# Performance work log

Hardware: AMD Instinct MI355X
Metric: run time of the kernel (lower is better)

## Reference

```python
import jax, jax.numpy as jnp
import numpy as np

N, F, K, D = 4096, 512, 8, 64
NEG_MIN = jnp.finfo(jnp.float32).min  # tf.float32.min used as additive mask


def setup_inputs() -> dict:
    key = jax.random.key(0)
    k1, k2, k3, k4, k5, k6 = jax.random.split(key, 6)
    H = jax.random.normal(k1, (N, F), dtype=jnp.float32)
    # binary adjacency as float (original multiplies (1 - A) by float32.min)
    A = jax.random.randint(k2, (N, N), 0, 2).astype(jnp.float32)
    idx = jnp.arange(N, dtype=jnp.int32)
    W = jax.random.normal(k3, (K, F, D), dtype=jnp.float32) * 0.05
    b = jax.random.normal(k4, (K, D), dtype=jnp.float32) * 0.05
    attn_k1 = jax.random.normal(k5, (K, D), dtype=jnp.float32) * 0.05
    attn_k2 = jax.random.normal(k6, (K, D), dtype=jnp.float32) * 0.05
    return {"H": H, "A": A, "idx": idx, "W": W, "b": b,
            "attn_k1": attn_k1, "attn_k2": attn_k2}


def reference(H, A, idx, W, b, attn_k1, attn_k2):
    # batch_A = gather(A, idx, axis=1); idx = arange(N) -> full adjacency
    batch_A = A[:, idx]                                   # [N, N]
    # all K heads at once (heads are independent, identical math)
    HW = jnp.einsum('nf,kfd->knd', H, W)                  # [K, N, D]
    s1 = jnp.einsum('knd,kd->kn', HW, attn_k1)            # [K, N]
    s2 = jnp.einsum('knd,kd->kn', HW, attn_k2)            # [K, N]
    # tf.meshgrid + transpose => attn[i, j] = s1[i] + s2[j]
    attn = s1[:, :, None] + s2[:, None, :]                # [K, N, N]
    attn = attn + NEG_MIN * (1.0 - batch_A)               # additive adjacency mask
    attn = jnp.where(attn > 0, attn, 0.2 * attn)          # LeakyReLU(0.2) AFTER mask
    attn = jax.nn.softmax(attn, axis=-1)                  # rows sum to 1
    # dropout layers are identity at inference (training=False)
    res = jnp.einsum('knm,kmd->knd', attn, HW) + b[:, None, :]
    res = jax.nn.relu(res)                                # activation per head (is_last=False)
    # concat heads along feature axis -> [N, K*D]
    return jnp.transpose(res, (1, 0, 2)).reshape(N, K * D)
```

## Files before the change

kernel.cpp:

```cpp
#include <hip/hip_runtime.h>
#include <hip/hip_bf16.h>

#define NN 4096
#define FF 512
#define KK 8
#define DD 64

typedef __attribute__((ext_vector_type(8))) short bf16x8;
typedef __attribute__((ext_vector_type(4))) float f32x4;

static __device__ __forceinline__ unsigned int cvt_pk_bf16(float lo, float hi) {
    unsigned int r;
    asm("v_cvt_pk_bf16_f32 %0, %1, %2" : "=v"(r) : "v"(lo), "v"(hi));
    return r;
}

__global__ __launch_bounds__(256) void pack_mask_k(const float* __restrict__ A,
                                                   unsigned int* __restrict__ Abits) {
    int w = blockIdx.x * 256 + threadIdx.x;
    const float4* src = (const float4*)(A + (size_t)w * 32);
    unsigned int bits = 0u;
#pragma unroll
    for (int i = 0; i < 8; ++i) {
        float4 v = src[i];
        bits |= (v.x != 0.f ? 1u : 0u) << (i * 4 + 0);
        bits |= (v.y != 0.f ? 1u : 0u) << (i * 4 + 1);
        bits |= (v.z != 0.f ? 1u : 0u) << (i * 4 + 2);
        bits |= (v.w != 0.f ? 1u : 0u) << (i * 4 + 3);
    }
    Abits[w] = bits;
}

__global__ __launch_bounds__(256) void cvt_h_k(const float* __restrict__ H,
                                               uint4* __restrict__ Hb4) {
    int i = blockIdx.x * 256 + threadIdx.x;
    float4 a = ((const float4*)H)[i * 2];
    float4 b = ((const float4*)H)[i * 2 + 1];
    uint4 v;
    v.x = cvt_pk_bf16(a.x, a.y);
    v.y = cvt_pk_bf16(a.z, a.w);
    v.z = cvt_pk_bf16(b.x, b.y);
    v.w = cvt_pk_bf16(b.z, b.w);
    Hb4[i] = v;
}

__global__ __launch_bounds__(256) void cvt_wt_k(const float* __restrict__ W,
                                                ushort* __restrict__ WT) {
    int k = blockIdx.x, f0 = blockIdx.y * 64;
    __shared__ float lds[64][65];
    const float* src = W + ((size_t)k * FF + f0) * DD;
    int t = threadIdx.x;
#pragma unroll
    for (int i = 0; i < 4; ++i) {
        int idx4 = t + i * 256;
        int f = idx4 >> 4, d4 = (idx4 & 15) * 4;
        float4 v = *(const float4*)(src + (size_t)f * DD + d4);
        lds[f][d4 + 0] = v.x; lds[f][d4 + 1] = v.y;
        lds[f][d4 + 2] = v.z; lds[f][d4 + 3] = v.w;
    }
    __syncthreads();
    int d = t >> 2, fs = (t & 3) * 16;
    ushort* dst = WT + ((size_t)k * DD + d) * FF + f0 + fs;
    uint4 v0, v1;
    v0.x = cvt_pk_bf16(lds[fs + 0][d], lds[fs + 1][d]);
    v0.y = cvt_pk_bf16(lds[fs + 2][d], lds[fs + 3][d]);
    v0.z = cvt_pk_bf16(lds[fs + 4][d], lds[fs + 5][d]);
    v0.w = cvt_pk_bf16(lds[fs + 6][d], lds[fs + 7][d]);
    v1.x = cvt_pk_bf16(lds[fs + 8][d], lds[fs + 9][d]);
    v1.y = cvt_pk_bf16(lds[fs + 10][d], lds[fs + 11][d]);
    v1.z = cvt_pk_bf16(lds[fs + 12][d], lds[fs + 13][d]);
    v1.w = cvt_pk_bf16(lds[fs + 14][d], lds[fs + 15][d]);
    *(uint4*)dst = v0;
    *(uint4*)(dst + 8) = v1;
}

__global__ __launch_bounds__(256) void hw_mfma_k(const ushort* __restrict__ Hb,
                                                 const ushort* __restrict__ WT,
                                                 const float* __restrict__ ak1,
                                                 const float* __restrict__ ak2,
                                                 float* __restrict__ r1,
                                                 float* __restrict__ E2,
                                                 float* __restrict__ e2p,
                                                 ushort* __restrict__ HWT2) {
    int k = blockIdx.x;
    int wrow = blockIdx.y * 64 + (threadIdx.x >> 6) * 16;
    int l = threadIdx.x & 63;
    int lr = l & 15, lg = l >> 4;

    f32x4 acc[4];
#pragma unroll
    for (int f = 0; f < 4; ++f) acc[f] = (f32x4){0.f, 0.f, 0.f, 0.f};

    const ushort* ha = Hb + (size_t)(wrow + lr) * FF + lg * 8;
    const ushort* wa = WT + (size_t)(k * DD + lr) * FF + lg * 8;
#pragma unroll 4
    for (int f0 = 0; f0 < FF; f0 += 32) {
        bf16x8 a = *(const bf16x8*)(ha + f0);
#pragma unroll
        for (int f = 0; f < 4; ++f) {
            bf16x8 b = *(const bf16x8*)(wa + (size_t)f * 16 * FF + f0);
            acc[f] = __builtin_amdgcn_mfma_f32_16x16x32_bf16(a, b, acc[f], 0, 0, 0);
        }
    }

    float p1[4] = {0.f, 0.f, 0.f, 0.f}, p2[4] = {0.f, 0.f, 0.f, 0.f};
#pragma unroll
    for (int f = 0; f < 4; ++f) {
        float a1 = ak1[k * DD + f * 16 + lr];
        float a2 = ak2[k * DD + f * 16 + lr];
#pragma unroll
        for (int i = 0; i < 4; ++i) {
            p1[i] = fmaf(acc[f][i], a1, p1[i]);
            p2[i] = fmaf(acc[f][i], a2, p2[i]);
        }
    }
#pragma unroll
    for (int off = 1; off < 16; off <<= 1) {
#pragma unroll
        for (int i = 0; i < 4; ++i) {
            p1[i] += __shfl_xor(p1[i], off);
            p2[i] += __shfl_xor(p2[i], off);
        }
    }
    if (lr == 0) {
#pragma unroll
        for (int i = 0; i < 4; ++i) {
            int n = k * NN + wrow + lg * 4 + i;
            r1[n]  = __expf(-0.8f * p1[i]);
            E2[n]  = __expf(p2[i]);
            e2p[n] = __expf(0.2f * p2[i]);
        }
    }
    size_t basei = ((size_t)(k * 512 + (wrow >> 3) + (lg >> 1))) * 512
                 + (size_t)lr * 8 + (lg & 1) * 4;
#pragma unroll
    for (int f = 0; f < 4; ++f) {
        uint2 v;
        v.x = cvt_pk_bf16(acc[f][0], acc[f][1]);
        v.y = cvt_pk_bf16(acc[f][2], acc[f][3]);
        *(uint2*)&HWT2[basei + (size_t)f * 128] = v;
    }
}

__global__ __launch_bounds__(256) void attn_pv_f(const ushort* __restrict__ HWT2,
                                                 const float* __restrict__ r1v,
                                                 const float* __restrict__ E2v,
                                                 const float* __restrict__ e2pv,
                                                 const unsigned char* __restrict__ Ab8,
                                                 const float* __restrict__ bias,
                                                 float* __restrict__ out) {
    int b = blockIdx.x;
    int k = b & 7;
    int row0 = (b >> 3) * 32;

    int w = threadIdx.x >> 6;
    int l = threadIdx.x & 63;
    int lr = l & 15, lg = l >> 4;

    __shared__ float tb[8192];
    __shared__ float ps[4][32];

    {
        const float4* e2s = (const float4*)(E2v + (size_t)k * NN);
        const float4* qps = (const float4*)(e2pv + (size_t)k * NN);
        float4* t4p = (float4*)tb;
#pragma unroll
        for (int n = 0; n < 4; ++n) {
            t4p[threadIdx.x + n * 256]        = e2s[threadIdx.x + n * 256];
            t4p[1024 + threadIdx.x + n * 256] = qps[threadIdx.x + n * 256];
        }
    }
    __syncthreads();

    float r1r0 = r1v[k * NN + row0 + lr];
    float r1r1 = r1v[k * NN + row0 + 16 + lr];
    const uint4* mrow0 = (const uint4*)(Ab8 + (size_t)(row0 + lr) * (NN / 8) + w * 128);
    const uint4* mrow1 = (const uint4*)(Ab8 + (size_t)(row0 + 16 + lr) * (NN / 8) + w * 128);
    const ushort* hwg = HWT2 + ((size_t)(k * 512 + w * 128 + lg)) * 512 + (size_t)lr * 8;
    const float* tE = tb + w * 1024 + lg * 8;
    const float* tQ = tb + 4096 + w * 1024 + lg * 8;

    bf16x8 onesb;
#pragma unroll
    for (int j = 0; j < 8; ++j) onesb[j] = (lr == 0) ? (short)0x3F80 : (short)0;

    f32x4 acc0[4], acc1[4];
#pragma unroll
    for (int f = 0; f < 4; ++f) {
        acc0[f] = (f32x4){0.f, 0.f, 0.f, 0.f};
        acc1[f] = (f32x4){0.f, 0.f, 0.f, 0.f};
    }
    f32x4 accs0 = (f32x4){0.f, 0.f, 0.f, 0.f};
    f32x4 accs1 = (f32x4){0.f, 0.f, 0.f, 0.f};

    bf16x8 bb[2][4];
#pragma unroll
    for (int f = 0; f < 4; ++f) bb[0][f] = *(const bf16x8*)(hwg + f * 128);

    for (int t4 = 0; t4 < 8; ++t4) {
        uint4 mu0 = mrow0[t4], mu1 = mrow1[t4];
        unsigned int mw0[4] = {mu0.x, mu0.y, mu0.z, mu0.w};
        unsigned int mw1[4] = {mu1.x, mu1.y, mu1.z, mu1.w};
#pragma unroll
        for (int j = 0; j < 4; ++j) {
            int it = t4 * 4 + j;
            const int cur = j & 1, nxt = cur ^ 1;
            int itn = it + 1 - ((it + 1) >> 5);
#pragma unroll
            for (int f = 0; f < 4; ++f)
                bb[nxt][f] = *(const bf16x8*)(hwg + (size_t)itn * 2048 + f * 128);
            const float* ltE = tE + it * 32;
            const float* ltQ = tQ + it * 32;
            float4 ea = *(const float4*)(ltE), eb = *(const float4*)(ltE + 4);
            float4 qa = *(const float4*)(ltQ), qb = *(const float4*)(ltQ + 4);
            float ev[8] = {ea.x, ea.y, ea.z, ea.w, eb.x, eb.y, eb.z, eb.w};
            float qv[8] = {qa.x, qa.y, qa.z, qa.w, qb.x, qb.y, qb.z, qb.w};
            unsigned int mb0 = (mw0[j] >> (lg * 8)) & 0xffu;
            unsigned int mb1 = (mw1[j] >> (lg * 8)) & 0xffu;
            uint4 au0, au1;
            unsigned int* pu0 = &au0.x;
            unsigned int* pu1 = &au1.x;
#pragma unroll
            for (int p = 0; p < 4; ++p) {
                int ja = 2 * p, jb = 2 * p + 1;
                unsigned int m0a = (unsigned int)(((int)(mb0 << (31 - ja))) >> 31);
                unsigned int m0b = (unsigned int)(((int)(mb0 << (31 - jb))) >> 31);
                unsigned int m1a = (unsigned int)(((int)(mb1 << (31 - ja))) >> 31);
                unsigned int m1b = (unsigned int)(((int)(mb1 << (31 - jb))) >> 31);
                float y0a = fmaxf(ev[ja], r1r0 * qv[ja]);
                float y0b = fmaxf(ev[jb], r1r0 * qv[jb]);
                float y1a = fmaxf(ev[ja], r1r1 * qv[ja]);
                float y1b = fmaxf(ev[jb], r1r1 * qv[jb]);
                y0a = __uint_as_float(__float_as_uint(y0a) & m0a);
                y0b = __uint_as_float(__float_as_uint(y0b) & m0b);
                y1a = __uint_as_float(__float_as_uint(y1a) & m1a);
                y1b = __uint_as_float(__float_as_uint(y1b) & m1b);
                pu0[p] = cvt_pk_bf16(y0a, y0b);
                pu1[p] = cvt_pk_bf16(y1a, y1b);
            }
            bf16x8 af0 = __builtin_bit_cast(bf16x8, au0);
            bf16x8 af1 = __builtin_bit_cast(bf16x8, au1);
            accs0 = __builtin_amdgcn_mfma_f32_16x16x32_bf16(af0, onesb, accs0, 0, 0, 0);
            accs1 = __builtin_amdgcn_mfma_f32_16x16x32_bf16(af1, onesb, accs1, 0, 0, 0);
#pragma unroll
            for (int f = 0; f < 4; ++f) {
                acc0[f] = __builtin_amdgcn_mfma_f32_16x16x32_bf16(af0, bb[cur][f], acc0[f], 0, 0, 0);
                acc1[f] = __builtin_amdgcn_mfma_f32_16x16x32_bf16(af1, bb[cur][f], acc1[f], 0, 0, 0);
            }
        }
    }

    __syncthreads();
#pragma unroll
    for (int f = 0; f < 4; ++f)
#pragma unroll
        for (int i = 0; i < 4; ++i) {
            tb[w * 2048 + (lg * 4 + i) * 64 + f * 16 + lr]      = acc0[f][i];
            tb[w * 2048 + (16 + lg * 4 + i) * 64 + f * 16 + lr] = acc1[f][i];
        }
    if (lr == 0) {
#pragma unroll
        for (int i = 0; i < 4; ++i) {
            ps[w][lg * 4 + i]      = accs0[i];
            ps[w][16 + lg * 4 + i] = accs1[i];
        }
    }
    __syncthreads();

    const float4* red4 = (const float4*)tb;
#pragma unroll
    for (int j2 = 0; j2 < 2; ++j2) {
        int o4 = threadIdx.x + j2 * 256;
        int row = o4 >> 4, d4 = (o4 & 15) * 4;
        float4 s0 = red4[o4], s1_ = red4[512 + o4];
        float4 s2_ = red4[1024 + o4], s3 = red4[1536 + o4];
        float rs = ps[0][row] + ps[1][row] + ps[2][row] + ps[3][row];
        float inv = 1.f / rs;
        float4 bi = *(const float4*)(bias + k * DD + d4);
        float4 o;
        o.x = fmaxf(fmaf(s0.x + s1_.x + s2_.x + s3.x, inv, bi.x), 0.f);
        o.y = fmaxf(fmaf(s0.y + s1_.y + s2_.y + s3.y, inv, bi.y), 0.f);
        o.z = fmaxf(fmaf(s0.z + s1_.z + s2_.z + s3.z, inv, bi.z), 0.f);
        o.w = fmaxf(fmaf(s0.w + s1_.w + s2_.w + s3.w, inv, bi.w), 0.f);
        *(float4*)&out[(size_t)(row0 + row) * (KK * DD) + k * DD + d4] = o;
    }
}

extern "C" void kernel_launch(void* const* d_in, const int* in_sizes, int n_in,
                              void* d_out, int out_size, void* d_ws, size_t ws_size,
                              hipStream_t stream) {
    const float* H   = (const float*)d_in[0];
    const float* A   = (const float*)d_in[1];
    const float* W   = (const float*)d_in[3];
    const float* b   = (const float*)d_in[4];
    const float* ak1 = (const float*)d_in[5];
    const float* ak2 = (const float*)d_in[6];
    float* out = (float*)d_out;

    char* ws = (char*)d_ws;
    size_t off = 0;
    ushort* Hb   = (ushort*)(ws + off); off += (size_t)NN * FF * 2;
    ushort* HWT2 = (ushort*)(ws + off); off += (size_t)KK * DD * NN * 2;
    ushort* WT   = (ushort*)(ws + off); off += (size_t)KK * DD * FF * 2;
    unsigned int* Abits = (unsigned int*)(ws + off); off += (size_t)NN * NN / 8;
    float* r1  = (float*)(ws + off); off += (size_t)KK * NN * 4;
    float* E2  = (float*)(ws + off); off += (size_t)KK * NN * 4;
    float* e2p = (float*)(ws + off); off += (size_t)KK * NN * 4;

    pack_mask_k<<<dim3(NN * (NN / 32) / 256), 256, 0, stream>>>(A, Abits);
    cvt_h_k<<<dim3(NN * FF / 8 / 256), 256, 0, stream>>>(H, (uint4*)Hb);
    cvt_wt_k<<<dim3(KK, FF / 64), 256, 0, stream>>>(W, WT);
    hw_mfma_k<<<dim3(KK, NN / 64), 256, 0, stream>>>(Hb, WT, ak1, ak2,
                                                     r1, E2, e2p, HWT2);
    attn_pv_f<<<dim3(KK * (NN / 32)), 256, 0, stream>>>(
        HWT2, r1, E2, e2p, (const unsigned char*)Abits, b, out);
}
```

Before: 78.29 us.

## Merge prep kernels into two launches and raise MFMA wave priority

Combines the H and W bf16 conversion kernels into one launch, and folds the adjacency bit-packing into the HW GEMM launch as extra blocks so the mask packing runs concurrently with the projection GEMM. This cuts launch count from five to three and lets the memory-bound mask pass overlap with compute-bound MFMA work. It also wraps the attention kernel's MFMA block with s_setprio to favor issuing matrix ops. Risks include block-level divergence in the merged kernels and scheduling interactions from the priority change.

```diff
diff --git a/kernel.cpp b/kernel.cpp
--- a/kernel.cpp
+++ b/kernel.cpp
@@ -15,75 +15,79 @@
     return r;
 }
 
-__global__ __launch_bounds__(256) void pack_mask_k(const float* __restrict__ A,
+__global__ __launch_bounds__(256) void prep_cvt_k(const float* __restrict__ H,
+                                                  const float* __restrict__ W,
+                                                  uint4* __restrict__ Hb4,
+                                                  ushort* __restrict__ WT) {
+    __shared__ float lds[64][65];
+    int bid = blockIdx.x;
+    int t = threadIdx.x;
+    if (bid < 1024) {
+        int i = bid * 256 + t;
+        float4 a = ((const float4*)H)[i * 2];
+        float4 b = ((const float4*)H)[i * 2 + 1];
+        uint4 v;
+        v.x = cvt_pk_bf16(a.x, a.y);
+        v.y = cvt_pk_bf16(a.z, a.w);
+        v.z = cvt_pk_bf16(b.x, b.y);
+        v.w = cvt_pk_bf16(b.z, b.w);
+        Hb4[i] = v;
+    } else {
+        int k = (bid - 1024) >> 3, f0 = ((bid - 1024) & 7) * 64;
+        const float* src = W + ((size_t)k * FF + f0) * DD;
+#pragma unroll
+        for (int i = 0; i < 4; ++i) {
+            int idx4 = t + i * 256;
+            int f = idx4 >> 4, d4 = (idx4 & 15) * 4;
+            float4 v = *(const float4*)(src + (size_t)f * DD + d4);
+            lds[f][d4 + 0] = v.x; lds[f][d4 + 1] = v.y;
+            lds[f][d4 + 2] = v.z; lds[f][d4 + 3] = v.w;
+        }
+        __syncthreads();
+        int d = t >> 2, fs = (t & 3) * 16;
+        ushort* dst = WT + ((size_t)k * DD + d) * FF + f0 + fs;
+        uint4 v0, v1;
+        v0.x = cvt_pk_bf16(lds[fs + 0][d], lds[fs + 1][d]);
+        v0.y = cvt_pk_bf16(lds[fs + 2][d], lds[fs + 3][d]);
+        v0.z = cvt_pk_bf16(lds[fs + 4][d], lds[fs + 5][d]);
+        v0.w = cvt_pk_bf16(lds[fs + 6][d], lds[fs + 7][d]);
+        v1.x = cvt_pk_bf16(lds[fs + 8][d], lds[fs + 9][d]);
+        v1.y = cvt_pk_bf16(lds[fs + 10][d], lds[fs + 11][d]);
+        v1.z = cvt_pk_bf16(lds[fs + 12][d], lds[fs + 13][d]);
+        v1.w = cvt_pk_bf16(lds[fs + 14][d], lds[fs + 15][d]);
+        *(uint4*)dst = v0;
+        *(uint4*)(dst + 8) = v1;
+    }
+}
+
+__global__ __launch_bounds__(256) void gemm_pack_k(const ushort* __restrict__ Hb,
+                                                   const ushort* __restrict__ WT,
+                                                   const float* __restrict__ ak1,
+                                                   const float* __restrict__ ak2,
+                                                   const float* __restrict__ A,
+                                                   float* __restrict__ r1,
+                                                   float* __restrict__ E2,
+                                                   float* __restrict__ e2p,
+                                                   ushort* __restrict__ HWT2,
                                                    unsigned int* __restrict__ Abits) {
-    int w = blockIdx.x * 256 + threadIdx.x;
-    const float4* src = (const float4*)(A + (size_t)w * 32);
-    unsigned int bits = 0u;
-#pragma unroll
-    for (int i = 0; i < 8; ++i) {
-        float4 v = src[i];
-        bits |= (v.x != 0.f ? 1u : 0u) << (i * 4 + 0);
-        bits |= (v.y != 0.f ? 1u : 0u) << (i * 4 + 1);
-        bits |= (v.z != 0.f ? 1u : 0u) << (i * 4 + 2);
-        bits |= (v.w != 0.f ? 1u : 0u) << (i * 4 + 3);
-    }
-    Abits[w] = bits;
-}
-
-__global__ __launch_bounds__(256) void cvt_h_k(const float* __restrict__ H,
-                                               uint4* __restrict__ Hb4) {
-    int i = blockIdx.x * 256 + threadIdx.x;
-    float4 a = ((const float4*)H)[i * 2];
-    float4 b = ((const float4*)H)[i * 2 + 1];
-    uint4 v;
-    v.x = cvt_pk_bf16(a.x, a.y);
-    v.y = cvt_pk_bf16(a.z, a.w);
-    v.z = cvt_pk_bf16(b.x, b.y);
-    v.w = cvt_pk_bf16(b.z, b.w);
-    Hb4[i] = v;
-}
-
-__global__ __launch_bounds__(256) void cvt_wt_k(const float* __restrict__ W,
-                                                ushort* __restrict__ WT) {
-    int k = blockIdx.x, f0 = blockIdx.y * 64;
-    __shared__ float lds[64][65];
-    const float* src = W + ((size_t)k * FF + f0) * DD;
-    int t = threadIdx.x;
-#pragma unroll
-    for (int i = 0; i < 4; ++i) {
-        int idx4 = t + i * 256;
-        int f = idx4 >> 4, d4 = (idx4 & 15) * 4;
-        float4 v = *(const float4*)(src + (size_t)f * DD + d4);
-        lds[f][d4 + 0] = v.x; lds[f][d4 + 1] = v.y;
-        lds[f][d4 + 2] = v.z; lds[f][d4 + 3] = v.w;
-    }
-    __syncthreads();
-    int d = t >> 2, fs = (t & 3) * 16;
-    ushort* dst = WT + ((size_t)k * DD + d) * FF + f0 + fs;
-    uint4 v0, v1;
-    v0.x = cvt_pk_bf16(lds[fs + 0][d], lds[fs + 1][d]);
-    v0.y = cvt_pk_bf16(lds[fs + 2][d], lds[fs + 3][d]);
-    v0.z = cvt_pk_bf16(lds[fs + 4][d], lds[fs + 5][d]);
-    v0.w = cvt_pk_bf16(lds[fs + 6][d], lds[fs + 7][d]);
-    v1.x = cvt_pk_bf16(lds[fs + 8][d], lds[fs + 9][d]);
-    v1.y = cvt_pk_bf16(lds[fs + 10][d], lds[fs + 11][d]);
-    v1.z = cvt_pk_bf16(lds[fs + 12][d], lds[fs + 13][d]);
-    v1.w = cvt_pk_bf16(lds[fs + 14][d], lds[fs + 15][d]);
-    *(uint4*)dst = v0;
-    *(uint4*)(dst + 8) = v1;
-}
-
-__global__ __launch_bounds__(256) void hw_mfma_k(const ushort* __restrict__ Hb,
-                                                 const ushort* __restrict__ WT,
-                                                 const float* __restrict__ ak1,
-                                                 const float* __restrict__ ak2,
-                                                 float* __restrict__ r1,
-                                                 float* __restrict__ E2,
-                                                 float* __restrict__ e2p,
-                                                 ushort* __restrict__ HWT2) {
-    int k = blockIdx.x;
-    int wrow = blockIdx.y * 64 + (threadIdx.x >> 6) * 16;
+    int bid = blockIdx.x;
+    if (bid >= 512) {
+        int w = (bid - 512) * 256 + threadIdx.x;
+        const float4* src = (const float4*)(A + (size_t)w * 32);
+        unsigned int bits = 0u;
+#pragma unroll
+        for (int i = 0; i < 8; ++i) {
+            float4 v = src[i];
+            bits |= (v.x != 0.f ? 1u : 0u) << (i * 4 + 0);
+            bits |= (v.y != 0.f ? 1u : 0u) << (i * 4 + 1);
+            bits |= (v.z != 0.f ? 1u : 0u) << (i * 4 + 2);
+            bits |= (v.w != 0.f ? 1u : 0u) << (i * 4 + 3);
+        }
+        Abits[w] = bits;
+        return;
+    }
+    int k = bid & 7;
+    int wrow = (bid >> 3) * 64 + (threadIdx.x >> 6) * 16;
     int l = threadIdx.x & 63;
     int lr = l & 15, lg = l >> 4;
 
@@ -240,6 +244,7 @@
             }
             bf16x8 af0 = __builtin_bit_cast(bf16x8, au0);
             bf16x8 af1 = __builtin_bit_cast(bf16x8, au1);
+            __builtin_amdgcn_s_setprio(1);
             accs0 = __builtin_amdgcn_mfma_f32_16x16x32_bf16(af0, onesb, accs0, 0, 0, 0);
             accs1 = __builtin_amdgcn_mfma_f32_16x16x32_bf16(af1, onesb, accs1, 0, 0, 0);
 #pragma unroll
@@ -247,6 +252,7 @@
                 acc0[f] = __builtin_amdgcn_mfma_f32_16x16x32_bf16(af0, bb[cur][f], acc0[f], 0, 0, 0);
                 acc1[f] = __builtin_amdgcn_mfma_f32_16x16x32_bf16(af1, bb[cur][f], acc1[f], 0, 0, 0);
             }
+            __builtin_amdgcn_s_setprio(0);
         }
     }
 
@@ -307,11 +313,9 @@
     float* E2  = (float*)(ws + off); off += (size_t)KK * NN * 4;
     float* e2p = (float*)(ws + off); off += (size_t)KK * NN * 4;
 
-    pack_mask_k<<<dim3(NN * (NN / 32) / 256), 256, 0, stream>>>(A, Abits);
-    cvt_h_k<<<dim3(NN * FF / 8 / 256), 256, 0, stream>>>(H, (uint4*)Hb);
-    cvt_wt_k<<<dim3(KK, FF / 64), 256, 0, stream>>>(W, WT);
-    hw_mfma_k<<<dim3(KK, NN / 64), 256, 0, stream>>>(Hb, WT, ak1, ak2,
-                                                     r1, E2, e2p, HWT2);
+    prep_cvt_k<<<dim3(1024 + 64), 256, 0, stream>>>(H, W, (uint4*)Hb, WT);
+    gemm_pack_k<<<dim3(512 + 2048), 256, 0, stream>>>(Hb, WT, ak1, ak2, A,
+                                                      r1, E2, e2p, HWT2, Abits);
     attn_pv_f<<<dim3(KK * (NN / 32)), 256, 0, stream>>>(
         HWT2, r1, E2, e2p, (const unsigned char*)Abits, b, out);
 }
```

After: 75.46 us. 3.6% less time.
